# Optimization experiments

Measured on AMD Instinct MI355X. Metric: run time of the kernel, lower is better.

The kernel has to match this reference:

```python
import jax, jax.numpy as jnp
import numpy as np

E = 8          # moe_num_experts
F = 4096       # ffn_hidden_size
D = 2048       # d_model
TOP_K = 2


def setup_inputs() -> dict:
    key = jax.random.key(0)
    k_x, k_r, k_w1, k_v1, k_w2 = jax.random.split(key, 5)
    scale = 0.02  # ~ normal initializer scale
    x = jax.random.normal(k_x, (2, 2048, D), dtype=jnp.float32)
    router_w = jax.random.normal(k_r, (D, E), dtype=jnp.float32) * scale
    w1 = jax.random.normal(k_w1, (E * F, D), dtype=jnp.float32) * scale
    v1 = jax.random.normal(k_v1, (E * F, D), dtype=jnp.float32) * scale
    w2 = jax.random.normal(k_w2, (E * F, D), dtype=jnp.float32) * scale
    return {"x": x, "router_w": router_w, "w1": w1, "v1": v1, "w2": w2}


def reference(x, router_w, w1, v1, w2):
    # --- Router: dense logits -> softmax (fp32) -> top-k -> L1 normalize ---
    logits = jnp.einsum("bsd,de->bse", x.astype(jnp.float32), router_w)
    weights = jax.nn.softmax(logits, axis=-1)                       # [B,S,E]
    top_weights, top_experts = jax.lax.top_k(weights, TOP_K)        # [B,S,K]
    # moe_normalize_expert_weights = 1 -> L1 norm
    top_weights = top_weights / jnp.sum(jnp.abs(top_weights), axis=-1, keepdims=True)
    top_weights = top_weights.astype(x.dtype)

    # --- Experts: dense per-expert GLU, masked combine (faithful to source) ---
    w1r = w1.reshape(E, F, D)
    v1r = v1.reshape(E, F, D)
    w2r = w2.reshape(E, F, D)
    out = jnp.zeros_like(x)
    for e in range(E):  # fixed small structural loop over experts
        x1 = jnp.einsum("bsd,fd->bsf", x, w1r[e])
        x2 = jnp.einsum("bsd,fd->bsf", x, v1r[e])
        h = jax.nn.silu(x1) * x2                                    # GLU
        y = jnp.einsum("bsf,fd->bsd", h, w2r[e])
        coef = jnp.sum((top_experts == e) * top_weights, axis=-1)[:, :, None]
        out = out + coef * y
    return out
```

## Files before the change

kernel.cpp:

```cpp
#include <hip/hip_runtime.h>
#include <cstdio>
#include <cstdint>

typedef _Float16 f16;
typedef _Float16 f16x8 __attribute__((ext_vector_type(8)));
typedef float f32x4 __attribute__((ext_vector_type(4)));

#define D_MODEL 2048
#define FFN     4096
#define FFN2    8192
#define NEXP    8
#define NTOK    4096
#define NENT    (NTOK*2)
#define BM      256
#define BN      256
#define BK      64
#define KSPLIT  4
#define KCHUNK  (FFN / KSPLIT)
#define MAX_ROWS  10240
#define MAX_TILES 40

__device__ __forceinline__ void gload_lds16(const void* g, void* l) {
  __builtin_amdgcn_global_load_lds(
      (const __attribute__((address_space(1))) void*)g,
      (__attribute__((address_space(3))) void*)l, 16, 0, 0);
}

template<int N> __device__ __forceinline__ void waitvm() {
  if constexpr (N == 0) asm volatile("s_waitcnt vmcnt(0)" ::: "memory");
  else if constexpr (N == 2) asm volatile("s_waitcnt vmcnt(2)" ::: "memory");
  else if constexpr (N == 4) asm volatile("s_waitcnt vmcnt(4)" ::: "memory");
  else if constexpr (N == 6) asm volatile("s_waitcnt vmcnt(6)" ::: "memory");
}

template<int LD>
__device__ __forceinline__ void stageA(const f16* aT, int k0, f16* AS, int mh, int tid) {
#pragma unroll
  for (int s = 0; s < 2; s++) {
    int o = s*8192 + tid*16;
    int rl = o >> 7;
    int ce = ((o & 127) ^ ((rl & 7) << 4)) >> 1;
    int arow = s*128 + mh*64 + (rl & 63);
    gload_lds16(aT + (size_t)arow * LD + k0 + ce,
                (char*)AS + mh*16384 + s*8192 + (tid & ~63)*16);
  }
}

template<int LD>
__device__ __forceinline__ void stageB(const f16* bT, int k0, f16* BS, int nh, int tid) {
#pragma unroll
  for (int s = 0; s < 2; s++) {
    int o = s*8192 + tid*16;
    int rl = o >> 7;
    int ce = ((o & 127) ^ ((rl & 7) << 4)) >> 1;
    int crow = (rl >> 5)*64 + nh*32 + (rl & 31);
    gload_lds16(bT + (size_t)crow * LD + k0 + ce,
                (char*)BS + nh*16384 + s*8192 + (tid & ~63)*16);
  }
}

__device__ __forceinline__ f16x8 fragLd(const f16* S, int row, int lane, int ks) {
  int kb = ks*64 + (lane >> 4)*16;
  int off = (row*128 + kb) ^ ((row & 7) << 4);
  return *(const f16x8*)((const char*)S + off);
}

template<int LD, int V0, int V1, int V3, bool SB0, bool SB1, bool SA1, bool SA0>
__device__ __forceinline__ void tile4(
    const f16* aT, const f16* bT, int k1, int k2,
    f16* ASc, f16* BSc, f16* ASn, f16* BSn,
    f32x4 (&acc)[8][4], f16x8 (&aF)[4][2], f16x8 (&bF)[2][2][2],
    int tid, int lane, int wrM, int wcN) {
#pragma unroll
  for (int mf = 0; mf < 4; mf++)
#pragma unroll
    for (int ks = 0; ks < 2; ks++)
      aF[mf][ks] = fragLd(ASc, wrM*64 + mf*16 + (lane & 15), lane, ks);
#pragma unroll
  for (int nf = 0; nf < 2; nf++)
#pragma unroll
    for (int ks = 0; ks < 2; ks++)
      bF[0][nf][ks] = fragLd(BSc, wcN*32 + nf*16 + (lane & 15), lane, ks);
  if constexpr (SB0) stageB<LD>(bT, k1, BSn, 0, tid);
  __builtin_amdgcn_s_barrier();
  __builtin_amdgcn_s_setprio(1);
#pragma unroll
  for (int mf = 0; mf < 4; mf++)
#pragma unroll
    for (int nf = 0; nf < 2; nf++)
#pragma unroll
      for (int ks = 0; ks < 2; ks++)
        acc[mf][nf] = __builtin_amdgcn_mfma_f32_16x16x32_f16(aF[mf][ks], bF[0][nf][ks], acc[mf][nf], 0, 0, 0);
  __builtin_amdgcn_s_setprio(0);
  waitvm<V0>();
  __builtin_amdgcn_s_barrier();
#pragma unroll
  for (int nf = 0; nf < 2; nf++)
#pragma unroll
    for (int ks = 0; ks < 2; ks++)
      bF[1][nf][ks] = fragLd(BSc, 128 + wcN*32 + nf*16 + (lane & 15), lane, ks);
  if constexpr (SB1) stageB<LD>(bT, k1, BSn, 1, tid);
  __builtin_amdgcn_s_barrier();
  __builtin_amdgcn_s_setprio(1);
#pragma unroll
  for (int mf = 0; mf < 4; mf++)
#pragma unroll
    for (int nf = 0; nf < 2; nf++)
#pragma unroll
      for (int ks = 0; ks < 2; ks++)
        acc[mf][2+nf] = __builtin_amdgcn_mfma_f32_16x16x32_f16(aF[mf][ks], bF[1][nf][ks], acc[mf][2+nf], 0, 0, 0);
  __builtin_amdgcn_s_setprio(0);
  waitvm<V1>();
  __builtin_amdgcn_s_barrier();
#pragma unroll
  for (int mf = 0; mf < 4; mf++)
#pragma unroll
    for (int ks = 0; ks < 2; ks++)
      aF[mf][ks] = fragLd(ASc, 128 + wrM*64 + mf*16 + (lane & 15), lane, ks);
  if constexpr (SA1) stageA<LD>(aT, k1, ASn, 1, tid);
  __builtin_amdgcn_s_barrier();
  __builtin_amdgcn_s_setprio(1);
#pragma unroll
  for (int mf = 0; mf < 4; mf++)
#pragma unroll
    for (int nf = 0; nf < 2; nf++)
#pragma unroll
      for (int ks = 0; ks < 2; ks++)
        acc[4+mf][nf] = __builtin_amdgcn_mfma_f32_16x16x32_f16(aF[mf][ks], bF[0][nf][ks], acc[4+mf][nf], 0, 0, 0);
  __builtin_amdgcn_s_setprio(0);
  __builtin_amdgcn_s_barrier();
  if constexpr (SA0) stageA<LD>(aT, k2, ASc, 0, tid);
  __builtin_amdgcn_s_barrier();
  __builtin_amdgcn_s_setprio(1);
#pragma unroll
  for (int mf = 0; mf < 4; mf++)
#pragma unroll
    for (int nf = 0; nf < 2; nf++)
#pragma unroll
      for (int ks = 0; ks < 2; ks++)
        acc[4+mf][2+nf] = __builtin_amdgcn_mfma_f32_16x16x32_f16(aF[mf][ks], bF[1][nf][ks], acc[4+mf][2+nf], 0, 0, 0);
  __builtin_amdgcn_s_setprio(0);
  waitvm<V3>();
  __builtin_amdgcn_s_barrier();
}


__global__ void zero_counts_kernel(int* counts) {
  if (threadIdx.x < NEXP) counts[threadIdx.x] = 0;
}

__global__ __launch_bounds__(64) void router_kernel(
    const float* __restrict__ x, const float* __restrict__ rw,
    int* counts, int* te, float* tw, int* trank) {
  int t = blockIdx.x;
  int lane = threadIdx.x;
  float acc[8] = {0.f,0.f,0.f,0.f,0.f,0.f,0.f,0.f};
  const float* xr = x + (size_t)t * D_MODEL;
  for (int d = lane; d < D_MODEL; d += 64) {
    float xv = xr[d];
    const float4* r4 = (const float4*)(rw + (size_t)d * NEXP);
    float4 a = r4[0], b = r4[1];
    acc[0] += xv*a.x; acc[1] += xv*a.y; acc[2] += xv*a.z; acc[3] += xv*a.w;
    acc[4] += xv*b.x; acc[5] += xv*b.y; acc[6] += xv*b.z; acc[7] += xv*b.w;
  }
#pragma unroll
  for (int off = 32; off > 0; off >>= 1) {
#pragma unroll
    for (int e = 0; e < 8; e++) acc[e] += __shfl_down(acc[e], off);
  }
  if (lane == 0) {
    int e0 = 0;
#pragma unroll
    for (int e = 1; e < 8; e++) if (acc[e] > acc[e0]) e0 = e;
    int e1 = (e0 == 0) ? 1 : 0;
#pragma unroll
    for (int e = 0; e < 8; e++) if (e != e0 && acc[e] > acc[e1]) e1 = e;
    float c0 = 1.0f / (1.0f + expf(acc[e1] - acc[e0]));
    float c1 = 1.0f - c0;
    int r0 = atomicAdd(&counts[e0], 1);
    int r1 = atomicAdd(&counts[e1], 1);
    te[t*2] = e0; te[t*2+1] = e1;
    tw[t*2] = c0; tw[t*2+1] = c1;
    trank[t*2] = r0; trank[t*2+1] = r1;
  }
}

__global__ void sched_kernel(const int* counts, int* offsets, int4* sched, int* nT) {
  if (threadIdx.x != 0 || blockIdx.x != 0) return;
  int off = 0, n = 0;
  for (int e = 0; e < NEXP; e++) {
    offsets[e] = off;
    int cnt = counts[e];
    int nt = (cnt + BM - 1) / BM;
    for (int i = 0; i < nt; i++) {
      sched[n] = make_int4(e, off + i*BM, min(BM, cnt - i*BM), 0);
      n++;
    }
    off += nt * BM;
  }
  offsets[NEXP] = off;
  *nT = n;
}

__global__ __launch_bounds__(256) void gather_kernel(
    const float* __restrict__ x, const int* __restrict__ te,
    const float* __restrict__ tw, const int* __restrict__ trank,
    const int* __restrict__ offsets, f16* __restrict__ xg,
    int* __restrict__ token_of, float* __restrict__ coefs) {
  int i = blockIdx.x;
  int t = i >> 1;
  int e = te[i];
  int slot = offsets[e] + trank[i];
  if (threadIdx.x == 0) { token_of[slot] = t; coefs[slot] = tw[i]; }
  const float4* src = (const float4*)(x + (size_t)t * D_MODEL);
  f16x8* dst = (f16x8*)(xg + (size_t)slot * D_MODEL);
  for (int j = threadIdx.x; j < D_MODEL/8; j += 256) {
    float4 v0 = src[j*2], v1 = src[j*2+1];
    f16x8 h;
    h[0]=(f16)v0.x; h[1]=(f16)v0.y; h[2]=(f16)v0.z; h[3]=(f16)v0.w;
    h[4]=(f16)v1.x; h[5]=(f16)v1.y; h[6]=(f16)v1.z; h[7]=(f16)v1.w;
    dst[j] = h;
  }
}

__global__ __launch_bounds__(256) void convert_both_kernel(
    const float* __restrict__ w1, const float* __restrict__ v1,
    f16* __restrict__ dst) {
  int n8 = NEXP*FFN*D_MODEL/8;
  int stride = gridDim.x * 256;
  for (int i = blockIdx.x*256 + threadIdx.x; i < n8; i += stride) {
    int d8 = i & (D_MODEL/8 - 1);
    int fr_glob = i >> 8;
    int e = fr_glob >> 12;
    int fr = fr_glob & (FFN - 1);
    int crbase = ((fr >> 4)*2)*16 + (fr & 15);
    float4 a0 = ((const float4*)w1)[(size_t)i*2];
    float4 a1 = ((const float4*)w1)[(size_t)i*2 + 1];
    float4 b0 = ((const float4*)v1)[(size_t)i*2];
    float4 b1 = ((const float4*)v1)[(size_t)i*2 + 1];
    f16x8 ha, hb;
    ha[0]=(f16)a0.x; ha[1]=(f16)a0.y; ha[2]=(f16)a0.z; ha[3]=(f16)a0.w;
    ha[4]=(f16)a1.x; ha[5]=(f16)a1.y; ha[6]=(f16)a1.z; ha[7]=(f16)a1.w;
    hb[0]=(f16)b0.x; hb[1]=(f16)b0.y; hb[2]=(f16)b0.z; hb[3]=(f16)b0.w;
    hb[4]=(f16)b1.x; hb[5]=(f16)b1.y; hb[6]=(f16)b1.z; hb[7]=(f16)b1.w;
    size_t base = ((size_t)e*FFN2 + crbase)*(D_MODEL/8) + d8;
    ((f16x8*)dst)[base] = ha;
    ((f16x8*)dst)[base + 16*(D_MODEL/8)] = hb;
  }
}

__global__ __launch_bounds__(256) void transpose_w2_kernel(
    const float* __restrict__ w2, f16* __restrict__ w2t) {
  __shared__ float tl[64][65];
  int e = blockIdx.z;
  int d0 = blockIdx.x * 64, f0 = blockIdx.y * 64;
  const float* src = w2 + (size_t)e * FFN * D_MODEL;
  int tid = threadIdx.x;
  int fr = tid >> 4, c4 = (tid & 15) * 4;
#pragma unroll
  for (int rr = 0; rr < 4; rr++) {
    float4 v = *(const float4*)(src + (size_t)(f0 + fr + rr*16) * D_MODEL + d0 + c4);
    tl[fr + rr*16][c4+0] = v.x; tl[fr + rr*16][c4+1] = v.y;
    tl[fr + rr*16][c4+2] = v.z; tl[fr + rr*16][c4+3] = v.w;
  }
  __syncthreads();
  int dr = tid >> 2, fg = (tid & 3) * 16;
  f16* dst = w2t + (size_t)e * D_MODEL * FFN + (size_t)(d0 + dr) * FFN + f0 + fg;
  f16 tmp[16];
#pragma unroll
  for (int j = 0; j < 16; j++) tmp[j] = (f16)tl[fg + j][dr];
  *(float4*)(dst)     = *(float4*)(tmp);
  *(float4*)(dst + 8) = *(float4*)(tmp + 8);
}

__global__ __launch_bounds__(512, 2) void phaseA_kernel(
    const f16* __restrict__ xg, const f16* __restrict__ w12h,
    f16* __restrict__ hbuf, const int4* __restrict__ sched, const int* __restrict__ nT) {
  int tile = blockIdx.y;
  if (tile >= *nT) return;
  int4 sc = sched[tile];
  int e = sc.x, row0 = sc.y;
  int fc0 = blockIdx.x * BN;

  __shared__ f16 AS[2][BM*BK];
  __shared__ f16 BS[2][BN*BK];

  int tid = threadIdx.x, lane = tid & 63, wid = tid >> 6;
  int wrM = wid >> 2, wcN = wid & 3;

  const f16* aT = xg  + (size_t)row0 * D_MODEL;
  const f16* bT = w12h + (size_t)e * FFN2 * D_MODEL + (size_t)fc0 * D_MODEL;

  f32x4 acc[8][4]; f16x8 aF[4][2]; f16x8 bF[2][2][2];
  f32x4 z4 = {0.f,0.f,0.f,0.f};
#pragma unroll
  for (int m = 0; m < 8; m++)
#pragma unroll
    for (int n = 0; n < 4; n++) acc[m][n] = z4;

  stageA<D_MODEL>(aT, 0, AS[0], 0, tid);
  stageB<D_MODEL>(bT, 0, BS[0], 0, tid);
  stageB<D_MODEL>(bT, 0, BS[0], 1, tid);
  stageA<D_MODEL>(aT, 0, AS[0], 1, tid);
  stageA<D_MODEL>(aT, BK, AS[1], 0, tid);
  waitvm<6>();
  __builtin_amdgcn_s_barrier();

  constexpr int NTILES = D_MODEL / BK;
  for (int t = 0; t + 2 < NTILES; t++) {
    int b = t & 1;
    tile4<D_MODEL,6,6,6,true,true,true,true>(aT, bT, (t+1)*BK, (t+2)*BK,
        AS[b], BS[b], AS[b^1], BS[b^1], acc, aF, bF, tid, lane, wrM, wcN);
  }
  { int b = (NTILES-2) & 1;
    tile4<D_MODEL,6,6,4,true,true,true,false>(aT, bT, (NTILES-1)*BK, 0,
        AS[b], BS[b], AS[b^1], BS[b^1], acc, aF, bF, tid, lane, wrM, wcN); }
  { int b = (NTILES-1) & 1;
    tile4<D_MODEL,2,0,-1,false,false,false,false>(aT, bT, 0, 0,
        AS[b], BS[b], AS[b^1], BS[b^1], acc, aF, bF, tid, lane, wrM, wcN); }

  int i15 = lane & 15, l4 = lane >> 4;
#pragma unroll
  for (int m = 0; m < 8; m++) {
    int rowl = wrM*128 + (m>>2)*64 + (m&3)*16 + l4*4;
#pragma unroll
    for (int nh = 0; nh < 2; nh++) {
      int f = (fc0 >> 1) + wcN*32 + nh*16 + i15;
      f16* hb = hbuf + (size_t)(row0 + rowl) * FFN + f;
#pragma unroll
      for (int q2 = 0; q2 < 4; q2++) {
        float x1 = acc[m][nh*2+0][q2], x2 = acc[m][nh*2+1][q2];
        float hv = x1 / (1.0f + __expf(-x1)) * x2;
        hb[(size_t)q2 * FFN] = (f16)hv;
      }
    }
  }
}

__global__ __launch_bounds__(512, 2) void phaseB_kernel(
    const f16* __restrict__ hbuf, const f16* __restrict__ w2t,
    f16* __restrict__ yb0, f16* __restrict__ ybR,
    const int4* __restrict__ sched, const int* __restrict__ nT) {
  int tile = blockIdx.y;
  if (tile >= *nT) return;
  int4 sc = sched[tile];
  int e = sc.x, row0 = sc.y;
  int dc0 = blockIdx.x * BN;
  int z = blockIdx.z;

  __shared__ f16 AS[2][BM*BK];
  __shared__ f16 BS[2][BN*BK];

  int tid = threadIdx.x, lane = tid & 63, wid = tid >> 6;
  int wrM = wid >> 2, wcN = wid & 3;

  const f16* aT = hbuf + (size_t)row0 * FFN + z * KCHUNK;
  const f16* bT = w2t + (size_t)e * D_MODEL * FFN + (size_t)dc0 * FFN + z * KCHUNK;

  f32x4 acc[8][4]; f16x8 aF[4][2]; f16x8 bF[2][2][2];
  f32x4 z4 = {0.f,0.f,0.f,0.f};
#pragma unroll
  for (int m = 0; m < 8; m++)
#pragma unroll
    for (int n = 0; n < 4; n++) acc[m][n] = z4;

  stageA<FFN>(aT, 0, AS[0], 0, tid);
  stageB<FFN>(bT, 0, BS[0], 0, tid);
  stageB<FFN>(bT, 0, BS[0], 1, tid);
  stageA<FFN>(aT, 0, AS[0], 1, tid);
  stageA<FFN>(aT, BK, AS[1], 0, tid);
  waitvm<6>();
  __builtin_amdgcn_s_barrier();

  constexpr int NTILES = KCHUNK / BK;
  for (int t = 0; t + 2 < NTILES; t++) {
    int b = t & 1;
    tile4<FFN,6,6,6,true,true,true,true>(aT, bT, (t+1)*BK, (t+2)*BK,
        AS[b], BS[b], AS[b^1], BS[b^1], acc, aF, bF, tid, lane, wrM, wcN);
  }
  { int b = (NTILES-2) & 1;
    tile4<FFN,6,6,4,true,true,true,false>(aT, bT, (NTILES-1)*BK, 0,
        AS[b], BS[b], AS[b^1], BS[b^1], acc, aF, bF, tid, lane, wrM, wcN); }
  { int b = (NTILES-1) & 1;
    tile4<FFN,2,0,-1,false,false,false,false>(aT, bT, 0, 0,
        AS[b], BS[b], AS[b^1], BS[b^1], acc, aF, bF, tid, lane, wrM, wcN); }

  f16* yb = (z == 0) ? yb0 : (ybR + (size_t)(z-1) * MAX_ROWS * D_MODEL);
  int i15 = lane & 15, l4 = lane >> 4;
#pragma unroll
  for (int m = 0; m < 8; m++) {
#pragma unroll
    for (int q2 = 0; q2 < 4; q2++) {
      int rl = wrM*128 + (m>>2)*64 + (m&3)*16 + l4*4 + q2;
      f16* yrow = yb + (size_t)(row0 + rl) * D_MODEL + dc0 + wcN*64;
#pragma unroll
      for (int n = 0; n < 4; n++)
        yrow[(n>>1)*32 + (n&1)*16 + i15] = (f16)acc[m][n][q2];
    }
  }
}

__global__ __launch_bounds__(256) void combine_kernel(
    const f16* __restrict__ yb0, const f16* __restrict__ ybR,
    const int* __restrict__ te, const float* __restrict__ tw,
    const int* __restrict__ trank, const int* __restrict__ offsets,
    float* __restrict__ out) {
  int t = blockIdx.x;
  int d8 = threadIdx.x;
  int s0 = offsets[te[2*t]]   + trank[2*t];
  int s1 = offsets[te[2*t+1]] + trank[2*t+1];
  float w0 = tw[2*t], w1 = tw[2*t+1];
  float sum[8] = {0.f,0.f,0.f,0.f,0.f,0.f,0.f,0.f};
#pragma unroll
  for (int z = 0; z < KSPLIT; z++) {
    const f16* yb = (z == 0) ? yb0 : (ybR + (size_t)(z-1) * MAX_ROWS * D_MODEL);
    f16x8 a = ((const f16x8*)(yb + (size_t)s0 * D_MODEL))[d8];
    f16x8 b = ((const f16x8*)(yb + (size_t)s1 * D_MODEL))[d8];
#pragma unroll
    for (int j = 0; j < 8; j++) sum[j] += w0 * (float)a[j] + w1 * (float)b[j];
  }
  float* o = out + (size_t)t * D_MODEL + d8*8;
  float4 o0 = {sum[0], sum[1], sum[2], sum[3]};
  float4 o1 = {sum[4], sum[5], sum[6], sum[7]};
  ((float4*)o)[0] = o0;
  ((float4*)o)[1] = o1;
}

extern "C" void kernel_launch(void* const* d_in, const int* in_sizes, int n_in,
                              void* d_out, int out_size, void* d_ws, size_t ws_size,
                              hipStream_t stream) {
  const float* x  = (const float*)d_in[0];
  const float* rw = (const float*)d_in[1];
  const float* w1 = (const float*)d_in[2];
  const float* v1 = (const float*)d_in[3];
  const float* w2 = (const float*)d_in[4];
  float* out = (float*)d_out;

  char* p = (char*)d_ws;
  auto alloc = [&](size_t bytes) {
    char* r = p;
    p += (bytes + 255) & ~(size_t)255;
    return r;
  };
  int*   counts   = (int*)  alloc(NEXP * 4);
  int*   nT       = (int*)  alloc(4);
  int*   offsets  = (int*)  alloc((NEXP + 1) * 4);
  int*   te       = (int*)  alloc(NENT * 4);
  float* tw       = (float*)alloc(NENT * 4);
  int*   trank    = (int*)  alloc(NENT * 4);
  int*   token_of = (int*)  alloc(MAX_ROWS * 4);
  float* coefs    = (float*)alloc(MAX_ROWS * 4);
  int4*  sched    = (int4*) alloc(MAX_TILES * 16);
  f16*   xg       = (f16*)  alloc((size_t)MAX_ROWS * D_MODEL * 2);
  f16*   hbuf     = (f16*)  alloc((size_t)MAX_ROWS * FFN * 2);
  f16*   w12h     = (f16*)  alloc((size_t)NEXP * FFN2 * D_MODEL * 2);
  f16*   w2t      = (f16*)  alloc((size_t)NEXP * FFN * D_MODEL * 2);
  size_t needed = (size_t)(p - (char*)d_ws);
  if (needed > ws_size) {
    fprintf(stderr, "kernel_launch: ws too small: need %zu, have %zu\n", needed, ws_size);
    return;
  }
  f16* yb0 = xg;
  f16* ybR = w12h;

  zero_counts_kernel<<<1, 64, 0, stream>>>(counts);
  router_kernel<<<NTOK, 64, 0, stream>>>(x, rw, counts, te, tw, trank);
  sched_kernel<<<1, 1, 0, stream>>>(counts, offsets, sched, nT);
  gather_kernel<<<NENT, 256, 0, stream>>>(x, te, tw, trank, offsets, xg, token_of, coefs);
  convert_both_kernel<<<4096, 256, 0, stream>>>(w1, v1, w12h);
  transpose_w2_kernel<<<dim3(D_MODEL/64, FFN/64, NEXP), 256, 0, stream>>>(w2, w2t);
  phaseA_kernel<<<dim3(FFN2/BN, MAX_TILES), 512, 0, stream>>>(xg, w12h, hbuf, sched, nT);
  phaseB_kernel<<<dim3(D_MODEL/BN, MAX_TILES, KSPLIT), 512, 0, stream>>>(hbuf, w2t, yb0, ybR, sched, nT);
  combine_kernel<<<NTOK, 256, 0, stream>>>(yb0, ybR, te, tw, trank, offsets, out);
}
```

Baseline: 895.5 us.

## Fuse fp32 w1/v1 to fp16 conversion into phaseA GEMM B-operand loading

Removes the separate convert_both pass that wrote an interleaved fp16 copy of w1/v1. phaseA now loads fp32 weight rows straight into registers, converts them to fp16 and writes them into swizzled LDS in the same layout. The loads for the next tile are issued during the MFMA phases so they overlap compute. This drops one full write and read of the fp16 weight copy, at the cost of more register pressure and redundant fp32 weight reads, since each weight tile is re-read by every row tile of the expert.

```diff
diff --git a/kernel.cpp b/kernel.cpp
--- a/kernel.cpp
+++ b/kernel.cpp
@@ -31,6 +31,15 @@
   else if constexpr (N == 2) asm volatile("s_waitcnt vmcnt(2)" ::: "memory");
   else if constexpr (N == 4) asm volatile("s_waitcnt vmcnt(4)" ::: "memory");
   else if constexpr (N == 6) asm volatile("s_waitcnt vmcnt(6)" ::: "memory");
+  else if constexpr (N == 8) asm volatile("s_waitcnt vmcnt(8)" ::: "memory");
+}
+
+__device__ __forceinline__ void lgkm0() {
+  asm volatile("s_waitcnt lgkmcnt(0)" ::: "memory");
+}
+
+__device__ __forceinline__ void gload4(f32x4& d, const float* p) {
+  asm volatile("global_load_dwordx4 %0, %1, off" : "=v"(d) : "v"(p));
 }
 
 template<int LD>
@@ -65,6 +74,96 @@
   return *(const f16x8*)((const char*)S + off);
 }
 
+__device__ __forceinline__ void quad(
+    f32x4 (&acc)[8][4], int mo, int no,
+    f16x8 (&aF)[4][2], f16x8 (&bFh)[2][2]) {
+#pragma unroll
+  for (int mf = 0; mf < 4; mf++)
+#pragma unroll
+    for (int nf = 0; nf < 2; nf++)
+#pragma unroll
+      for (int ks = 0; ks < 2; ks++)
+        acc[mo+mf][no+nf] = __builtin_amdgcn_mfma_f32_16x16x32_f16(
+            aF[mf][ks], bFh[nf][ks], acc[mo+mf][no+nf], 0, 0, 0);
+}
+
+template<bool SA, bool CV, bool IB, int VEND>
+__device__ __forceinline__ void tile4A(
+    const f16* aT, int k1, int k2,
+    f16* ASc, f16* BSc, f16* ASn, f16* BSn,
+    f32x4 (&acc)[8][4], f32x4 (&br)[8],
+    const float* const (&gb)[4], const int (&lo)[4],
+    int tid, int lane, int wrM, int wcN) {
+  f16x8 aF[4][2]; f16x8 bF[2][2][2];
+  int i15 = lane & 15;
+#pragma unroll
+  for (int mf = 0; mf < 4; mf++)
+#pragma unroll
+    for (int ks = 0; ks < 2; ks++)
+      aF[mf][ks] = fragLd(ASc, wrM*64 + mf*16 + i15, lane, ks);
+#pragma unroll
+  for (int nf = 0; nf < 2; nf++)
+#pragma unroll
+    for (int ks = 0; ks < 2; ks++)
+      bF[0][nf][ks] = fragLd(BSc, wcN*32 + nf*16 + i15, lane, ks);
+  __builtin_amdgcn_s_barrier();
+  __builtin_amdgcn_s_setprio(1);
+  quad(acc, 0, 0, aF, bF[0]);
+  __builtin_amdgcn_s_setprio(0);
+  __builtin_amdgcn_s_barrier();
+#pragma unroll
+  for (int nf = 0; nf < 2; nf++)
+#pragma unroll
+    for (int ks = 0; ks < 2; ks++)
+      bF[1][nf][ks] = fragLd(BSc, 128 + wcN*32 + nf*16 + i15, lane, ks);
+  if constexpr (SA) {
+    stageA<D_MODEL>(aT, k1, ASn, 0, tid);
+    stageA<D_MODEL>(aT, k1, ASn, 1, tid);
+  }
+  __builtin_amdgcn_s_barrier();
+  __builtin_amdgcn_s_setprio(1);
+  quad(acc, 0, 2, aF, bF[1]);
+  __builtin_amdgcn_s_setprio(0);
+  __builtin_amdgcn_s_barrier();
+#pragma unroll
+  for (int mf = 0; mf < 4; mf++)
+#pragma unroll
+    for (int ks = 0; ks < 2; ks++)
+      aF[mf][ks] = fragLd(ASc, 128 + wrM*64 + mf*16 + i15, lane, ks);
+  if constexpr (CV) {
+    waitvm<4>();
+    __builtin_amdgcn_sched_barrier(0);
+#pragma unroll
+    for (int s = 0; s < 4; s++) {
+      f16x8 h;
+      h[0]=(f16)br[2*s][0]; h[1]=(f16)br[2*s][1];
+      h[2]=(f16)br[2*s][2]; h[3]=(f16)br[2*s][3];
+      h[4]=(f16)br[2*s+1][0]; h[5]=(f16)br[2*s+1][1];
+      h[6]=(f16)br[2*s+1][2]; h[7]=(f16)br[2*s+1][3];
+      *(f16x8*)((char*)BSn + lo[s]) = h;
+    }
+  }
+  __builtin_amdgcn_s_barrier();
+  __builtin_amdgcn_s_setprio(1);
+  quad(acc, 4, 0, aF, bF[0]);
+  __builtin_amdgcn_s_setprio(0);
+  __builtin_amdgcn_s_barrier();
+  if constexpr (IB) {
+#pragma unroll
+    for (int s = 0; s < 4; s++) {
+      gload4(br[2*s],   gb[s] + k2);
+      gload4(br[2*s+1], gb[s] + k2 + 4);
+    }
+  }
+  __builtin_amdgcn_s_barrier();
+  __builtin_amdgcn_s_setprio(1);
+  quad(acc, 4, 2, aF, bF[1]);
+  __builtin_amdgcn_s_setprio(0);
+  if constexpr (CV) lgkm0();
+  waitvm<VEND>();
+  __builtin_amdgcn_s_barrier();
+}
+
 template<int LD, int V0, int V1, int V3, bool SB0, bool SB1, bool SA1, bool SA0>
 __device__ __forceinline__ void tile4(
     const f16* aT, const f16* bT, int k1, int k2,
@@ -84,13 +183,7 @@
   if constexpr (SB0) stageB<LD>(bT, k1, BSn, 0, tid);
   __builtin_amdgcn_s_barrier();
   __builtin_amdgcn_s_setprio(1);
-#pragma unroll
-  for (int mf = 0; mf < 4; mf++)
-#pragma unroll
-    for (int nf = 0; nf < 2; nf++)
-#pragma unroll
-      for (int ks = 0; ks < 2; ks++)
-        acc[mf][nf] = __builtin_amdgcn_mfma_f32_16x16x32_f16(aF[mf][ks], bF[0][nf][ks], acc[mf][nf], 0, 0, 0);
+  quad(acc, 0, 0, aF, bF[0]);
   __builtin_amdgcn_s_setprio(0);
   waitvm<V0>();
   __builtin_amdgcn_s_barrier();
@@ -102,13 +195,7 @@
   if constexpr (SB1) stageB<LD>(bT, k1, BSn, 1, tid);
   __builtin_amdgcn_s_barrier();
   __builtin_amdgcn_s_setprio(1);
-#pragma unroll
-  for (int mf = 0; mf < 4; mf++)
-#pragma unroll
-    for (int nf = 0; nf < 2; nf++)
-#pragma unroll
-      for (int ks = 0; ks < 2; ks++)
-        acc[mf][2+nf] = __builtin_amdgcn_mfma_f32_16x16x32_f16(aF[mf][ks], bF[1][nf][ks], acc[mf][2+nf], 0, 0, 0);
+  quad(acc, 0, 2, aF, bF[1]);
   __builtin_amdgcn_s_setprio(0);
   waitvm<V1>();
   __builtin_amdgcn_s_barrier();
@@ -120,25 +207,13 @@
   if constexpr (SA1) stageA<LD>(aT, k1, ASn, 1, tid);
   __builtin_amdgcn_s_barrier();
   __builtin_amdgcn_s_setprio(1);
-#pragma unroll
-  for (int mf = 0; mf < 4; mf++)
-#pragma unroll
-    for (int nf = 0; nf < 2; nf++)
-#pragma unroll
-      for (int ks = 0; ks < 2; ks++)
-        acc[4+mf][nf] = __builtin_amdgcn_mfma_f32_16x16x32_f16(aF[mf][ks], bF[0][nf][ks], acc[4+mf][nf], 0, 0, 0);
+  quad(acc, 4, 0, aF, bF[0]);
   __builtin_amdgcn_s_setprio(0);
   __builtin_amdgcn_s_barrier();
   if constexpr (SA0) stageA<LD>(aT, k2, ASc, 0, tid);
   __builtin_amdgcn_s_barrier();
   __builtin_amdgcn_s_setprio(1);
-#pragma unroll
-  for (int mf = 0; mf < 4; mf++)
-#pragma unroll
-    for (int nf = 0; nf < 2; nf++)
-#pragma unroll
-      for (int ks = 0; ks < 2; ks++)
-        acc[4+mf][2+nf] = __builtin_amdgcn_mfma_f32_16x16x32_f16(aF[mf][ks], bF[1][nf][ks], acc[4+mf][2+nf], 0, 0, 0);
+  quad(acc, 4, 2, aF, bF[1]);
   __builtin_amdgcn_s_setprio(0);
   waitvm<V3>();
   __builtin_amdgcn_s_barrier();
@@ -223,32 +298,6 @@
   }
 }
 
-__global__ __launch_bounds__(256) void convert_both_kernel(
-    const float* __restrict__ w1, const float* __restrict__ v1,
-    f16* __restrict__ dst) {
-  int n8 = NEXP*FFN*D_MODEL/8;
-  int stride = gridDim.x * 256;
-  for (int i = blockIdx.x*256 + threadIdx.x; i < n8; i += stride) {
-    int d8 = i & (D_MODEL/8 - 1);
-    int fr_glob = i >> 8;
-    int e = fr_glob >> 12;
-    int fr = fr_glob & (FFN - 1);
-    int crbase = ((fr >> 4)*2)*16 + (fr & 15);
-    float4 a0 = ((const float4*)w1)[(size_t)i*2];
-    float4 a1 = ((const float4*)w1)[(size_t)i*2 + 1];
-    float4 b0 = ((const float4*)v1)[(size_t)i*2];
-    float4 b1 = ((const float4*)v1)[(size_t)i*2 + 1];
-    f16x8 ha, hb;
-    ha[0]=(f16)a0.x; ha[1]=(f16)a0.y; ha[2]=(f16)a0.z; ha[3]=(f16)a0.w;
-    ha[4]=(f16)a1.x; ha[5]=(f16)a1.y; ha[6]=(f16)a1.z; ha[7]=(f16)a1.w;
-    hb[0]=(f16)b0.x; hb[1]=(f16)b0.y; hb[2]=(f16)b0.z; hb[3]=(f16)b0.w;
-    hb[4]=(f16)b1.x; hb[5]=(f16)b1.y; hb[6]=(f16)b1.z; hb[7]=(f16)b1.w;
-    size_t base = ((size_t)e*FFN2 + crbase)*(D_MODEL/8) + d8;
-    ((f16x8*)dst)[base] = ha;
-    ((f16x8*)dst)[base + 16*(D_MODEL/8)] = hb;
-  }
-}
-
 __global__ __launch_bounds__(256) void transpose_w2_kernel(
     const float* __restrict__ w2, f16* __restrict__ w2t) {
   __shared__ float tl[64][65];
@@ -274,7 +323,8 @@
 }
 
 __global__ __launch_bounds__(512, 2) void phaseA_kernel(
-    const f16* __restrict__ xg, const f16* __restrict__ w12h,
+    const f16* __restrict__ xg, const float* __restrict__ w1,
+    const float* __restrict__ v1,
     f16* __restrict__ hbuf, const int4* __restrict__ sched, const int* __restrict__ nT) {
   int tile = blockIdx.y;
   if (tile >= *nT) return;
@@ -288,10 +338,24 @@
   int tid = threadIdx.x, lane = tid & 63, wid = tid >> 6;
   int wrM = wid >> 2, wcN = wid & 3;
 
-  const f16* aT = xg  + (size_t)row0 * D_MODEL;
-  const f16* bT = w12h + (size_t)e * FFN2 * D_MODEL + (size_t)fc0 * D_MODEL;
-
-  f32x4 acc[8][4]; f16x8 aF[4][2]; f16x8 bF[2][2][2];
+  const f16* aT = xg + (size_t)row0 * D_MODEL;
+
+  const float* gb[4];
+  int lo[4];
+#pragma unroll
+  for (int s = 0; s < 4; s++) {
+    int nh = s >> 1;
+    int rl = ((s & 1)*512 + tid) >> 3;
+    int c0f = (tid & 7) * 8;
+    int crow = (rl >> 5)*64 + nh*32 + (rl & 31);
+    int sel = (crow >> 4) & 1;
+    int frl = ((crow >> 5) << 4) | (crow & 15);
+    const float* base = sel ? v1 : w1;
+    gb[s] = base + ((size_t)e * FFN + (fc0 >> 1) + frl) * D_MODEL + c0f;
+    lo[s] = nh*16384 + ((rl*128 + c0f*2) ^ ((rl & 7) << 4));
+  }
+
+  f32x4 acc[8][4]; f32x4 br[8];
   f32x4 z4 = {0.f,0.f,0.f,0.f};
 #pragma unroll
   for (int m = 0; m < 8; m++)
@@ -299,25 +363,37 @@
     for (int n = 0; n < 4; n++) acc[m][n] = z4;
 
   stageA<D_MODEL>(aT, 0, AS[0], 0, tid);
-  stageB<D_MODEL>(bT, 0, BS[0], 0, tid);
-  stageB<D_MODEL>(bT, 0, BS[0], 1, tid);
   stageA<D_MODEL>(aT, 0, AS[0], 1, tid);
-  stageA<D_MODEL>(aT, BK, AS[1], 0, tid);
-  waitvm<6>();
+#pragma unroll
+  for (int s = 0; s < 4; s++) { gload4(br[2*s], gb[s]); gload4(br[2*s+1], gb[s]+4); }
+  waitvm<0>();
+  __builtin_amdgcn_sched_barrier(0);
+#pragma unroll
+  for (int s = 0; s < 4; s++) {
+    f16x8 h;
+    h[0]=(f16)br[2*s][0]; h[1]=(f16)br[2*s][1];
+    h[2]=(f16)br[2*s][2]; h[3]=(f16)br[2*s][3];
+    h[4]=(f16)br[2*s+1][0]; h[5]=(f16)br[2*s+1][1];
+    h[6]=(f16)br[2*s+1][2]; h[7]=(f16)br[2*s+1][3];
+    *(f16x8*)((char*)BS[0] + lo[s]) = h;
+  }
+#pragma unroll
+  for (int s = 0; s < 4; s++) { gload4(br[2*s], gb[s]+BK); gload4(br[2*s+1], gb[s]+BK+4); }
+  lgkm0();
   __builtin_amdgcn_s_barrier();
 
   constexpr int NTILES = D_MODEL / BK;
-  for (int t = 0; t + 2 < NTILES; t++) {
+  for (int t = 0; t < NTILES - 2; t++) {
     int b = t & 1;
-    tile4<D_MODEL,6,6,6,true,true,true,true>(aT, bT, (t+1)*BK, (t+2)*BK,
-        AS[b], BS[b], AS[b^1], BS[b^1], acc, aF, bF, tid, lane, wrM, wcN);
+    tile4A<true,true,true,8>(aT, (t+1)*BK, (t+2)*BK,
+        AS[b], BS[b], AS[b^1], BS[b^1], acc, br, gb, lo, tid, lane, wrM, wcN);
   }
   { int b = (NTILES-2) & 1;
-    tile4<D_MODEL,6,6,4,true,true,true,false>(aT, bT, (NTILES-1)*BK, 0,
-        AS[b], BS[b], AS[b^1], BS[b^1], acc, aF, bF, tid, lane, wrM, wcN); }
+    tile4A<true,true,false,0>(aT, (NTILES-1)*BK, 0,
+        AS[b], BS[b], AS[b^1], BS[b^1], acc, br, gb, lo, tid, lane, wrM, wcN); }
   { int b = (NTILES-1) & 1;
-    tile4<D_MODEL,2,0,-1,false,false,false,false>(aT, bT, 0, 0,
-        AS[b], BS[b], AS[b^1], BS[b^1], acc, aF, bF, tid, lane, wrM, wcN); }
+    tile4A<false,false,false,-1>(aT, 0, 0,
+        AS[b], BS[b], AS[b^1], BS[b^1], acc, br, gb, lo, tid, lane, wrM, wcN); }
 
   int i15 = lane & 15, l4 = lane >> 4;
 #pragma unroll
@@ -453,7 +529,7 @@
   int4*  sched    = (int4*) alloc(MAX_TILES * 16);
   f16*   xg       = (f16*)  alloc((size_t)MAX_ROWS * D_MODEL * 2);
   f16*   hbuf     = (f16*)  alloc((size_t)MAX_ROWS * FFN * 2);
-  f16*   w12h     = (f16*)  alloc((size_t)NEXP * FFN2 * D_MODEL * 2);
+  f16*   ybR      = (f16*)  alloc((size_t)(KSPLIT-1) * MAX_ROWS * D_MODEL * 2);
   f16*   w2t      = (f16*)  alloc((size_t)NEXP * FFN * D_MODEL * 2);
   size_t needed = (size_t)(p - (char*)d_ws);
   if (needed > ws_size) {
@@ -461,15 +537,13 @@
     return;
   }
   f16* yb0 = xg;
-  f16* ybR = w12h;
 
   zero_counts_kernel<<<1, 64, 0, stream>>>(counts);
   router_kernel<<<NTOK, 64, 0, stream>>>(x, rw, counts, te, tw, trank);
   sched_kernel<<<1, 1, 0, stream>>>(counts, offsets, sched, nT);
   gather_kernel<<<NENT, 256, 0, stream>>>(x, te, tw, trank, offsets, xg, token_of, coefs);
-  convert_both_kernel<<<4096, 256, 0, stream>>>(w1, v1, w12h);
   transpose_w2_kernel<<<dim3(D_MODEL/64, FFN/64, NEXP), 256, 0, stream>>>(w2, w2t);
-  phaseA_kernel<<<dim3(FFN2/BN, MAX_TILES), 512, 0, stream>>>(xg, w12h, hbuf, sched, nT);
+  phaseA_kernel<<<dim3(FFN2/BN, MAX_TILES), 512, 0, stream>>>(xg, w1, v1, hbuf, sched, nT);
   phaseB_kernel<<<dim3(D_MODEL/BN, MAX_TILES, KSPLIT), 512, 0, stream>>>(hbuf, w2t, yb0, ybR, sched, nT);
   combine_kernel<<<NTOK, 256, 0, stream>>>(yb0, ybR, te, tw, trank, offsets, out);
 }
```

After: 1.162 ms. 1.3x slower.
